# Performance work log

Measured on AMD Instinct MI355X. Metric: run time of the kernel, lower is better.

The kernel has to match this reference:

```python
import jax, jax.numpy as jnp
from jax import lax
import numpy as np

B, C, H, Wd = 32, 128, 56, 56
FILTERS = 128
KH = KW = 3
T_MIN_PREV = 0.0  # module defaults (set_params never called)
T_MIN = 0.0
T_MAX = 1.0


def setup_inputs() -> dict:
    key = jax.random.key(0)
    k1, k2 = jax.random.split(key)
    tj = jax.random.uniform(k1, (B, C, H, Wd), dtype=jnp.float32)          # spike times
    W = jax.random.normal(k2, (C * KH * KW, FILTERS), dtype=jnp.float32) * 0.02  # kernel.view(-1, filters)
    D_i = jnp.zeros((9, FILTERS), dtype=jnp.float32)                        # intrinsic delays (only row 0 used)
    return {"tj": tj, "W": W, "D_i": D_i}


def reference(tj, W, D_i):
    # 'same' padding with value t_min, then unfold + (tj - t_min) @ W is
    # exactly a zero-padded conv on (tj - t_min): the pad entries become 0.
    x = tj - T_MIN                                   # [B,C,H,W]
    # Unfold orders patch rows as (C, kh, kw); build the equivalent OIHW kernel.
    kernel = jnp.transpose(W.reshape(C, KH, KW, FILTERS), (3, 0, 1, 2))  # [F,C,KH,KW]
    y = lax.conv_general_dilated(
        x, kernel, window_strides=(1, 1), padding="SAME",
        dimension_numbers=("NCHW", "OIHW", "NCHW"))    # [B,F,H,W]
    threshold = T_MAX - T_MIN - D_i[0]                 # [F]
    ti = y + threshold[None, :, None, None] + T_MIN
    ti = jnp.minimum(ti, T_MAX)                        # torch.where(ti < t_max, ti, t_max)
    return jnp.transpose(ti, (0, 2, 3, 1))             # [B,H,W,F], matches ti.view(b,H,W,filters)
```

## Files before the change

kernel.cpp:

```cpp
#include <hip/hip_runtime.h>


#define BZ 32
#define CC 128
#define HH 56
#define WWD 56
#define HWP 3136
#define FF 128
#define KT 9
#define PH 58
#define PW 58
#define MTOT 100352
#define BM 128

typedef __attribute__((ext_vector_type(8))) __bf16 bf16x8;
typedef __attribute__((ext_vector_type(4))) float f32x4;
typedef __attribute__((ext_vector_type(8))) unsigned short us8;
typedef __attribute__((ext_vector_type(4))) float flt4;

__device__ __forceinline__ unsigned short f2bf(float f) {
  unsigned int u = __float_as_uint(f);
  unsigned int r = (u + 0x7FFFu + ((u >> 16) & 1u)) >> 16;
  return (unsigned short)r;
}

#define GLOAD_LDS16(g, l)                                                              \
  __builtin_amdgcn_global_load_lds((const __attribute__((address_space(1))) void*)(g), \
                                   (__attribute__((address_space(3))) void*)(l), 16, 0, 0)

__global__ void prep_w_kernel(const float* __restrict__ W, unsigned short* __restrict__ Wt,
                              int swz) {
  int idx = blockIdx.x * 256 + threadIdx.x;
  if (idx >= KT * FF * CC) return;
  int r = idx >> 14;
  int rem = idx & 16383;
  int f = rem >> 7;
  int c = rem & 127;
  int cs = swz ? (c ^ ((f & 7) << 3)) : c;
  Wt[(r * FF + f) * CC + cs] = f2bf(W[(c * KT + r) * FF + f]);
}

__global__ __launch_bounds__(256) void prep_x_kernel(const float* __restrict__ x,
                                                     unsigned short* __restrict__ xp) {
  const int blk = blockIdx.x;
  const int b = blk / PH;
  const int ph = blk - b * PH;
  const int tid = threadIdx.x;
  unsigned short* dst = xp + (size_t)(b * PH + ph) * PW * CC;

  if (ph == 0 || ph == PH - 1) {
    us8 z;
#pragma unroll
    for (int k = 0; k < 8; ++k) z[k] = 0;
    for (int i = tid; i < PW * CC / 8; i += 256) reinterpret_cast<us8*>(dst)[i] = z;
    return;
  }

  __shared__ float sm[CC][57];
  const int h = ph - 1;
  {
    const int c = tid >> 1;
    const int half = tid & 1;
    const float* src = x + ((size_t)(b * CC + c)) * HWP + h * WWD + half * 28;
#pragma unroll
    for (int k = 0; k < 7; ++k) {
      flt4 v = *reinterpret_cast<const flt4*>(src + k * 4);
      sm[c][half * 28 + k * 4 + 0] = v[0];
      sm[c][half * 28 + k * 4 + 1] = v[1];
      sm[c][half * 28 + k * 4 + 2] = v[2];
      sm[c][half * 28 + k * 4 + 3] = v[3];
    }
  }
  __syncthreads();
  for (int i = tid; i < PW * 16; i += 256) {
    const int ww = i >> 4;
    const int cg = i & 15;
    us8 v;
    if (ww == 0 || ww == PW - 1) {
#pragma unroll
      for (int k = 0; k < 8; ++k) v[k] = 0;
    } else {
      const int w = ww - 1;
#pragma unroll
      for (int k = 0; k < 8; ++k) v[k] = f2bf(sm[cg * 8 + k][w]);
    }
    reinterpret_cast<us8*>(dst)[i] = v;
  }
}

__global__ __launch_bounds__(256, 2) void spiking_conv_main(
    const unsigned short* __restrict__ xp, const unsigned short* __restrict__ Wt,
    const float* __restrict__ Di, float* __restrict__ out) {
  __shared__ unsigned short Asm[BM * CC];
  __shared__ unsigned short Bsm[FF * CC];

  const int bid = blockIdx.x;
  const int wg = (bid & 7) * 98 + (bid >> 3);
  const int m0 = wg * BM;

  const int tid = threadIdx.x;
  const int lane = tid & 63;
  const int wv = tid >> 6;
  const int wr = wv >> 1, wc = wv & 1;
  const int frow = lane & 15, kg = lane >> 4;

  int aoff[8];
#pragma unroll
  for (int t = 0; t < 8; ++t) {
    const int row = wv * 32 + t * 4 + (lane >> 4);
    const int m = m0 + row;
    const int b = m / HWP;
    const int p = m - b * HWP;
    const int h = p / WWD;
    const int w = p - h * WWD;
    const int chunk = (lane & 15) ^ (row & 7);
    aoff[t] = ((b * PH + h + 1) * PW + (w + 1)) * CC + chunk * 8;
  }
  const unsigned short* wsrc = Wt + wv * 4096 + lane * 8;

  f32x4 acc[4][4];
  const f32x4 zero = {0.0f, 0.0f, 0.0f, 0.0f};
#pragma unroll
  for (int i = 0; i < 4; ++i)
#pragma unroll
    for (int j = 0; j < 4; ++j) acc[i][j] = zero;

  for (int r = 0; r < KT; ++r) {
    const int dh = r / 3 - 1;
    const int dw = r - (r / 3) * 3 - 1;
    const int tapoff = (dh * PW + dw) * CC;
    __syncthreads();
#pragma unroll
    for (int t = 0; t < 8; ++t)
      GLOAD_LDS16(xp + aoff[t] + tapoff, Asm + wv * 4096 + t * 512);
#pragma unroll
    for (int t = 0; t < 8; ++t)
      GLOAD_LDS16(wsrc + r * (FF * CC) + t * 512, Bsm + wv * 4096 + t * 512);
    __syncthreads();

#pragma unroll
    for (int kk = 0; kk < 4; ++kk) {
      bf16x8 af[4], bfr[4];
#pragma unroll
      for (int i = 0; i < 4; ++i) {
        const int rowA = wr * 64 + i * 16 + frow;
        const int colb = (kk * 64 + kg * 16) ^ ((rowA & 7) << 4);
        af[i] = *reinterpret_cast<const bf16x8*>(
            reinterpret_cast<const char*>(Asm) + rowA * 256 + colb);
      }
#pragma unroll
      for (int j = 0; j < 4; ++j) {
        const int rowB = wc * 64 + j * 16 + frow;
        const int colb = (kk * 64 + kg * 16) ^ ((rowB & 7) << 4);
        bfr[j] = *reinterpret_cast<const bf16x8*>(
            reinterpret_cast<const char*>(Bsm) + rowB * 256 + colb);
      }
#pragma unroll
      for (int i = 0; i < 4; ++i)
#pragma unroll
        for (int j = 0; j < 4; ++j)
          acc[i][j] = __builtin_amdgcn_mfma_f32_16x16x32_bf16(af[i], bfr[j], acc[i][j], 0, 0, 0);
    }
  }

#pragma unroll
  for (int j = 0; j < 4; ++j) {
    const int col = wc * 64 + j * 16 + frow;
    const float thr = 1.0f - Di[col];
#pragma unroll
    for (int i = 0; i < 4; ++i) {
      const int rbase = m0 + wr * 64 + i * 16 + kg * 4;
#pragma unroll
      for (int q = 0; q < 4; ++q) {
        float v = acc[i][j][q] + thr;
        out[(size_t)(rbase + q) * FF + col] = fminf(v, 1.0f);
      }
    }
  }
}

__global__ __launch_bounds__(256) void spiking_conv_fallback(
    const float* __restrict__ x, const unsigned short* __restrict__ Wt,
    const float* __restrict__ Wf, const float* __restrict__ Di,
    float* __restrict__ out, int useWt) {
  __shared__ unsigned short Asm2[BM][32];
  __shared__ unsigned short Bsm2[FF][32];
  const int tid = threadIdx.x;
  const int m0 = blockIdx.x * BM;
  const int mi = tid & 127;
  const int half = tid >> 7;
  const int m = m0 + mi;
  const int bimg = m / HWP;
  const int p = m - bimg * HWP;
  const int h = p / WWD;
  const int w = p - h * WWD;
  const int baseA = (bimg * CC) * HWP + h * WWD + w;
  const int lane = tid & 63;
  const int wid = tid >> 6;
  const int wr = wid >> 1;
  const int wc = wid & 1;
  const int frow = lane & 15;
  const int kg = lane >> 4;
  f32x4 acc[4][4];
  const f32x4 zero = {0.0f, 0.0f, 0.0f, 0.0f};
#pragma unroll
  for (int i = 0; i < 4; ++i)
#pragma unroll
    for (int j = 0; j < 4; ++j) acc[i][j] = zero;
  for (int r = 0; r < KT; ++r) {
    const int dh = r / 3 - 1;
    const int dw = r - (r / 3) * 3 - 1;
    const int hh = h + dh;
    const int ww2 = w + dw;
    const bool valid = ((unsigned)hh < (unsigned)HH) && ((unsigned)ww2 < (unsigned)WWD);
    const int aoff2 = baseA + dh * WWD + dw + half * 16 * HWP;
    for (int c0 = 0; c0 < CC; c0 += 32) {
      __syncthreads();
      {
        const float* src = x + aoff2 + c0 * HWP;
        us8 v0, v1;
#pragma unroll
        for (int i = 0; i < 8; ++i) {
          float f0 = valid ? src[i * HWP] : 0.0f;
          float f1 = valid ? src[(i + 8) * HWP] : 0.0f;
          v0[i] = f2bf(f0);
          v1[i] = f2bf(f1);
        }
        *reinterpret_cast<us8*>(&Asm2[mi][half * 16]) = v0;
        *reinterpret_cast<us8*>(&Asm2[mi][half * 16 + 8]) = v1;
      }
      if (useWt) {
        const unsigned short* src = Wt + (r * FF + mi) * CC + c0 + half * 16;
        *reinterpret_cast<us8*>(&Bsm2[mi][half * 16]) = *reinterpret_cast<const us8*>(src);
        *reinterpret_cast<us8*>(&Bsm2[mi][half * 16 + 8]) = *reinterpret_cast<const us8*>(src + 8);
      } else {
        us8 v0, v1;
#pragma unroll
        for (int i = 0; i < 8; ++i) {
          int c = c0 + half * 16 + i;
          v0[i] = f2bf(Wf[(c * KT + r) * FF + mi]);
          v1[i] = f2bf(Wf[((c + 8) * KT + r) * FF + mi]);
        }
        *reinterpret_cast<us8*>(&Bsm2[mi][half * 16]) = v0;
        *reinterpret_cast<us8*>(&Bsm2[mi][half * 16 + 8]) = v1;
      }
      __syncthreads();
      bf16x8 af[4], bfr[4];
#pragma unroll
      for (int i = 0; i < 4; ++i)
        af[i] = *reinterpret_cast<const bf16x8*>(&Asm2[wr * 64 + i * 16 + frow][kg * 8]);
#pragma unroll
      for (int j = 0; j < 4; ++j)
        bfr[j] = *reinterpret_cast<const bf16x8*>(&Bsm2[wc * 64 + j * 16 + frow][kg * 8]);
#pragma unroll
      for (int i = 0; i < 4; ++i)
#pragma unroll
        for (int j = 0; j < 4; ++j)
          acc[i][j] = __builtin_amdgcn_mfma_f32_16x16x32_bf16(af[i], bfr[j], acc[i][j], 0, 0, 0);
    }
  }
#pragma unroll
  for (int j = 0; j < 4; ++j) {
    const int col = wc * 64 + j * 16 + frow;
    const float thr = 1.0f - Di[col];
#pragma unroll
    for (int i = 0; i < 4; ++i) {
      const int rbase = m0 + wr * 64 + i * 16 + kg * 4;
#pragma unroll
      for (int q = 0; q < 4; ++q) {
        float v = acc[i][j][q] + thr;
        out[(size_t)(rbase + q) * FF + col] = fminf(v, 1.0f);
      }
    }
  }
}

extern "C" void kernel_launch(void* const* d_in, const int* in_sizes, int n_in,
                              void* d_out, int out_size, void* d_ws, size_t ws_size,
                              hipStream_t stream) {
  const float* tj = (const float*)d_in[0];
  const float* W = (const float*)d_in[1];
  const float* Di = (const float*)d_in[2];
  float* out = (float*)d_out;

  const size_t wt_bytes = (size_t)KT * FF * CC * 2;
  const size_t xp_bytes = (size_t)BZ * PH * PW * CC * 2;
  unsigned short* Wt = (unsigned short*)d_ws;
  unsigned short* xp = (unsigned short*)((char*)d_ws + wt_bytes);

  if (ws_size >= wt_bytes + xp_bytes) {
    prep_w_kernel<<<(KT * FF * CC + 255) / 256, 256, 0, stream>>>(W, Wt, 1);
    prep_x_kernel<<<BZ * PH, 256, 0, stream>>>(tj, xp);
    spiking_conv_main<<<MTOT / BM, 256, 0, stream>>>(xp, Wt, Di, out);
  } else {
    const int useWt = (ws_size >= wt_bytes) ? 1 : 0;
    if (useWt) prep_w_kernel<<<(KT * FF * CC + 255) / 256, 256, 0, stream>>>(W, Wt, 0);
    spiking_conv_fallback<<<MTOT / BM, 256, 0, stream>>>(tj, Wt, W, Di, out, useWt);
  }
}
```

Baseline: 66.15 us.

## Tile conv by spatial row blocks with shared halo patch and pipelined K-steps

The main conv kernel now assigns each 512-thread workgroup an 8-row spatial tile of one image. It loads one padded halo patch per 32-channel quarter into LDS and reuses it for all 9 taps by shifting addresses, instead of reloading A for every tap. Weights are re-laid out per (quarter, tap) step and double-buffered. The 36 steps are fully unrolled via templates, with prefetch of the next step overlapped with MFMA. This cuts redundant global A traffic and barrier stalls, at the cost of 96KB dynamic LDS, a large accumulator register footprint (7x4 tiles), and only 224 workgroups.

New measurement: 58.40 us. 1.13x faster.

```diff
diff --git a/kernel.cpp b/kernel.cpp
--- a/kernel.cpp
+++ b/kernel.cpp
@@ -7,11 +7,15 @@
 #define WWD 56
 #define HWP 3136
 #define FF 128
-#define KT 9
 #define PH 58
 #define PW 58
-#define MTOT 100352
-#define BM 128
+#define QC 32
+#define PATCH_G 2320
+#define PATCH_BYTES 40960
+#define BQ_OFF 81920
+#define BQ_BYTES 8192
+#define LDS_TOTAL 98304
+#define NSTEP 36
 
 typedef __attribute__((ext_vector_type(8))) __bf16 bf16x8;
 typedef __attribute__((ext_vector_type(4))) float f32x4;
@@ -28,16 +32,21 @@
   __builtin_amdgcn_global_load_lds((const __attribute__((address_space(1))) void*)(g), \
                                    (__attribute__((address_space(3))) void*)(l), 16, 0, 0)
 
-__global__ void prep_w_kernel(const float* __restrict__ W, unsigned short* __restrict__ Wt,
-                              int swz) {
+__global__ void prep_w_kernel(const float* __restrict__ W, unsigned short* __restrict__ Wt) {
   int idx = blockIdx.x * 256 + threadIdx.x;
-  if (idx >= KT * FF * CC) return;
-  int r = idx >> 14;
-  int rem = idx & 16383;
-  int f = rem >> 7;
-  int c = rem & 127;
-  int cs = swz ? (c ^ ((f & 7) << 3)) : c;
-  Wt[(r * FF + f) * CC + cs] = f2bf(W[(c * KT + r) * FF + f]);
+  if (idx >= 4 * 9 * 512) return;
+  int qr = idx >> 9;
+  int gp = idx & 511;
+  int g = gp ^ ((gp >> 3) & 7);
+  int q = qr / 9, r = qr - q * 9;
+  int f = g >> 2, kg = g & 3;
+  us8 v;
+#pragma unroll
+  for (int j = 0; j < 8; ++j) {
+    int c = q * QC + kg * 8 + j;
+    v[j] = f2bf(W[(c * 9 + r) * FF + f]);
+  }
+  *reinterpret_cast<us8*>(Wt + (size_t)idx * 8) = v;
 }
 
 __global__ __launch_bounds__(256) void prep_x_kernel(const float* __restrict__ x,
@@ -88,105 +97,155 @@
   }
 }
 
-__global__ __launch_bounds__(256, 2) void spiking_conv_main(
+struct Ctx {
+  const unsigned short* xp;
+  const unsigned short* Wt;
+  int tid;
+  int srcA[5];
+  int gbase[7];
+  int bOffB[4];
+  f32x4 acc[7][4];
+};
+
+template <int S>
+__device__ __forceinline__ void step(Ctx& c, unsigned char* lds) {
+  constexpr int q = S / 9, r = S - q * 9;
+  constexpr int dh = r / 3 - 1, dw = r - (r / 3) * 3 - 1;
+  constexpr int tapoff = dh * 232 + dw * 4;
+  constexpr bool issueA = (r < 5) && (q < 3);
+  constexpr bool issueB = (S < NSTEP - 1);
+  constexpr int nIssue = (issueA ? 1 : 0) + (issueB ? 1 : 0);
+
+  if constexpr (issueA) {
+    const unsigned short* src = c.xp + c.srcA[r] + (q + 1) * QC;
+    unsigned char* dst = lds + ((q + 1) & 1) * PATCH_BYTES + (size_t)(r * 512 + c.tid) * 16;
+    GLOAD_LDS16(src, dst);
+  }
+  if constexpr (issueB) {
+    const unsigned short* src = c.Wt + (size_t)(S + 1) * 4096 + c.tid * 8;
+    unsigned char* dst = lds + BQ_OFF + ((S + 1) & 1) * BQ_BYTES + (size_t)c.tid * 16;
+    GLOAD_LDS16(src, dst);
+  }
+  asm volatile("s_waitcnt vmcnt(%0)" ::"n"(nIssue));
+  __builtin_amdgcn_s_barrier();
+  __builtin_amdgcn_sched_barrier(0);
+
+  const unsigned char* pa = lds + (q & 1) * PATCH_BYTES;
+  const unsigned char* pb = lds + BQ_OFF + (S & 1) * BQ_BYTES;
+  bf16x8 af[7], bf[4];
+#pragma unroll
+  for (int i = 0; i < 7; ++i) {
+    int g = c.gbase[i] + tapoff;
+    int ga = (g ^ ((g >> 3) & 7)) << 4;
+    af[i] = *reinterpret_cast<const bf16x8*>(pa + ga);
+  }
+#pragma unroll
+  for (int j = 0; j < 4; ++j)
+    bf[j] = *reinterpret_cast<const bf16x8*>(pb + c.bOffB[j]);
+
+  __builtin_amdgcn_s_setprio(1);
+#pragma unroll
+  for (int i = 0; i < 7; ++i)
+#pragma unroll
+    for (int j = 0; j < 4; ++j)
+      c.acc[i][j] = __builtin_amdgcn_mfma_f32_16x16x32_bf16(af[i], bf[j], c.acc[i][j], 0, 0, 0);
+  __builtin_amdgcn_s_setprio(0);
+  __builtin_amdgcn_sched_barrier(0);
+  __builtin_amdgcn_s_barrier();
+}
+
+template <int S>
+__device__ __forceinline__ void do_steps(Ctx& c, unsigned char* lds) {
+  step<S>(c, lds);
+  if constexpr (S + 1 < NSTEP) do_steps<S + 1>(c, lds);
+}
+
+__global__ __launch_bounds__(512, 2) void spiking_conv_main(
     const unsigned short* __restrict__ xp, const unsigned short* __restrict__ Wt,
     const float* __restrict__ Di, float* __restrict__ out) {
-  __shared__ unsigned short Asm[BM * CC];
-  __shared__ unsigned short Bsm[FF * CC];
+  extern __shared__ unsigned char lds[];
 
   const int bid = blockIdx.x;
-  const int wg = (bid & 7) * 98 + (bid >> 3);
-  const int m0 = wg * BM;
-
+  const int wg = (bid & 7) * 28 + (bid >> 3);
+  const int b = wg / 7;
+  const int ht = wg - b * 7;
+  const int h0 = ht * 8;
+
+  Ctx c;
+  c.xp = xp;
+  c.Wt = Wt;
   const int tid = threadIdx.x;
-  const int lane = tid & 63;
-  const int wv = tid >> 6;
+  c.tid = tid;
+  const int lane = tid & 63, wv = tid >> 6;
   const int wr = wv >> 1, wc = wv & 1;
   const int frow = lane & 15, kg = lane >> 4;
 
-  int aoff[8];
-#pragma unroll
-  for (int t = 0; t < 8; ++t) {
-    const int row = wv * 32 + t * 4 + (lane >> 4);
-    const int m = m0 + row;
-    const int b = m / HWP;
-    const int p = m - b * HWP;
-    const int h = p / WWD;
-    const int w = p - h * WWD;
-    const int chunk = (lane & 15) ^ (row & 7);
-    aoff[t] = ((b * PH + h + 1) * PW + (w + 1)) * CC + chunk * 8;
-  }
-  const unsigned short* wsrc = Wt + wv * 4096 + lane * 8;
-
-  f32x4 acc[4][4];
+#pragma unroll
+  for (int k = 0; k < 5; ++k) {
+    int gp = k * 512 + tid;
+    int g = gp ^ ((gp >> 3) & 7);
+    int ph = g / 232;
+    int rem = g - ph * 232;
+    int pw = rem >> 2;
+    int kg2 = rem & 3;
+    int e = ((b * PH + h0 + ph) * PW + pw) * CC + kg2 * 8;
+    c.srcA[k] = (gp < PATCH_G) ? e : 0;
+  }
+#pragma unroll
+  for (int i = 0; i < 7; ++i) {
+    int t = 16 * i + frow;
+    int hl = (t >= 56) ? 1 : 0;
+    int wl = t - 56 * hl;
+    c.gbase[i] = ((2 * wr + hl + 1) * 58 + (wl + 1)) * 4 + kg;
+  }
+#pragma unroll
+  for (int j = 0; j < 4; ++j) {
+    int gB = (wc * 64 + 16 * j + frow) * 4 + kg;
+    c.bOffB[j] = (gB ^ ((gB >> 3) & 7)) << 4;
+  }
   const f32x4 zero = {0.0f, 0.0f, 0.0f, 0.0f};
 #pragma unroll
-  for (int i = 0; i < 4; ++i)
-#pragma unroll
-    for (int j = 0; j < 4; ++j) acc[i][j] = zero;
-
-  for (int r = 0; r < KT; ++r) {
-    const int dh = r / 3 - 1;
-    const int dw = r - (r / 3) * 3 - 1;
-    const int tapoff = (dh * PW + dw) * CC;
-    __syncthreads();
-#pragma unroll
-    for (int t = 0; t < 8; ++t)
-      GLOAD_LDS16(xp + aoff[t] + tapoff, Asm + wv * 4096 + t * 512);
-#pragma unroll
-    for (int t = 0; t < 8; ++t)
-      GLOAD_LDS16(wsrc + r * (FF * CC) + t * 512, Bsm + wv * 4096 + t * 512);
-    __syncthreads();
-
-#pragma unroll
-    for (int kk = 0; kk < 4; ++kk) {
-      bf16x8 af[4], bfr[4];
-#pragma unroll
-      for (int i = 0; i < 4; ++i) {
-        const int rowA = wr * 64 + i * 16 + frow;
-        const int colb = (kk * 64 + kg * 16) ^ ((rowA & 7) << 4);
-        af[i] = *reinterpret_cast<const bf16x8*>(
-            reinterpret_cast<const char*>(Asm) + rowA * 256 + colb);
+  for (int i = 0; i < 7; ++i)
+#pragma unroll
+    for (int j = 0; j < 4; ++j) c.acc[i][j] = zero;
+
+#pragma unroll
+  for (int k = 0; k < 5; ++k)
+    GLOAD_LDS16(xp + c.srcA[k], lds + (size_t)(k * 512 + tid) * 16);
+  GLOAD_LDS16(Wt + tid * 8, lds + BQ_OFF + (size_t)tid * 16);
+  asm volatile("s_waitcnt vmcnt(0)");
+  __builtin_amdgcn_s_barrier();
+  __builtin_amdgcn_sched_barrier(0);
+
+  do_steps<0>(c, lds);
+
+#pragma unroll
+  for (int j = 0; j < 4; ++j) {
+    const int col = wc * 64 + 16 * j + frow;
+    const float thr = 1.0f - Di[col];
+#pragma unroll
+    for (int i = 0; i < 7; ++i) {
+      const int bt = 16 * i + kg * 4;
+      const int hl = (bt >= 56) ? 1 : 0;
+      const int wl0 = bt - 56 * hl;
+      const int orow = h0 + 2 * wr + hl;
+      const size_t obase = ((size_t)b * HWP + (size_t)orow * WWD + wl0) * FF + col;
+#pragma unroll
+      for (int qq = 0; qq < 4; ++qq) {
+        float v = c.acc[i][j][qq] + thr;
+        out[obase + (size_t)qq * FF] = fminf(v, 1.0f);
       }
-#pragma unroll
-      for (int j = 0; j < 4; ++j) {
-        const int rowB = wc * 64 + j * 16 + frow;
-        const int colb = (kk * 64 + kg * 16) ^ ((rowB & 7) << 4);
-        bfr[j] = *reinterpret_cast<const bf16x8*>(
-            reinterpret_cast<const char*>(Bsm) + rowB * 256 + colb);
-      }
-#pragma unroll
-      for (int i = 0; i < 4; ++i)
-#pragma unroll
-        for (int j = 0; j < 4; ++j)
-          acc[i][j] = __builtin_amdgcn_mfma_f32_16x16x32_bf16(af[i], bfr[j], acc[i][j], 0, 0, 0);
-    }
-  }
-
-#pragma unroll
-  for (int j = 0; j < 4; ++j) {
-    const int col = wc * 64 + j * 16 + frow;
-    const float thr = 1.0f - Di[col];
-#pragma unroll
-    for (int i = 0; i < 4; ++i) {
-      const int rbase = m0 + wr * 64 + i * 16 + kg * 4;
-#pragma unroll
-      for (int q = 0; q < 4; ++q) {
-        float v = acc[i][j][q] + thr;
-        out[(size_t)(rbase + q) * FF + col] = fminf(v, 1.0f);
-      }
     }
   }
 }
 
 __global__ __launch_bounds__(256) void spiking_conv_fallback(
-    const float* __restrict__ x, const unsigned short* __restrict__ Wt,
-    const float* __restrict__ Wf, const float* __restrict__ Di,
-    float* __restrict__ out, int useWt) {
-  __shared__ unsigned short Asm2[BM][32];
-  __shared__ unsigned short Bsm2[FF][32];
+    const float* __restrict__ x, const float* __restrict__ Wf,
+    const float* __restrict__ Di, float* __restrict__ out) {
+  __shared__ unsigned short Asm2[128][32];
+  __shared__ unsigned short Bsm2[128][32];
   const int tid = threadIdx.x;
-  const int m0 = blockIdx.x * BM;
+  const int m0 = blockIdx.x * 128;
   const int mi = tid & 127;
   const int half = tid >> 7;
   const int m = m0 + mi;
@@ -207,7 +266,7 @@
   for (int i = 0; i < 4; ++i)
 #pragma unroll
     for (int j = 0; j < 4; ++j) acc[i][j] = zero;
-  for (int r = 0; r < KT; ++r) {
+  for (int r = 0; r < 9; ++r) {
     const int dh = r / 3 - 1;
     const int dw = r - (r / 3) * 3 - 1;
     const int hh = h + dh;
@@ -229,17 +288,13 @@
         *reinterpret_cast<us8*>(&Asm2[mi][half * 16]) = v0;
         *reinterpret_cast<us8*>(&Asm2[mi][half * 16 + 8]) = v1;
       }
-      if (useWt) {
-        const unsigned short* src = Wt + (r * FF + mi) * CC + c0 + half * 16;
-        *reinterpret_cast<us8*>(&Bsm2[mi][half * 16]) = *reinterpret_cast<const us8*>(src);
-        *reinterpret_cast<us8*>(&Bsm2[mi][half * 16 + 8]) = *reinterpret_cast<const us8*>(src + 8);
-      } else {
+      {
         us8 v0, v1;
 #pragma unroll
         for (int i = 0; i < 8; ++i) {
-          int c = c0 + half * 16 + i;
-          v0[i] = f2bf(Wf[(c * KT + r) * FF + mi]);
-          v1[i] = f2bf(Wf[((c + 8) * KT + r) * FF + mi]);
+          int cc2 = c0 + half * 16 + i;
+          v0[i] = f2bf(Wf[(cc2 * 9 + r) * FF + mi]);
+          v1[i] = f2bf(Wf[((cc2 + 8) * 9 + r) * FF + mi]);
         }
         *reinterpret_cast<us8*>(&Bsm2[mi][half * 16]) = v0;
         *reinterpret_cast<us8*>(&Bsm2[mi][half * 16 + 8]) = v1;
@@ -267,9 +322,9 @@
     for (int i = 0; i < 4; ++i) {
       const int rbase = m0 + wr * 64 + i * 16 + kg * 4;
 #pragma unroll
-      for (int q = 0; q < 4; ++q) {
-        float v = acc[i][j][q] + thr;
-        out[(size_t)(rbase + q) * FF + col] = fminf(v, 1.0f);
+      for (int qq = 0; qq < 4; ++qq) {
+        float v = acc[i][j][qq] + thr;
+        out[(size_t)(rbase + qq) * FF + col] = fminf(v, 1.0f);
       }
     }
   }
@@ -283,18 +338,19 @@
   const float* Di = (const float*)d_in[2];
   float* out = (float*)d_out;
 
-  const size_t wt_bytes = (size_t)KT * FF * CC * 2;
+  const size_t wt_bytes = (size_t)4 * 9 * 512 * 16;
   const size_t xp_bytes = (size_t)BZ * PH * PW * CC * 2;
   unsigned short* Wt = (unsigned short*)d_ws;
   unsigned short* xp = (unsigned short*)((char*)d_ws + wt_bytes);
 
-  if (ws_size >= wt_bytes + xp_bytes) {
-    prep_w_kernel<<<(KT * FF * CC + 255) / 256, 256, 0, stream>>>(W, Wt, 1);
+  bool fast = (ws_size >= wt_bytes + xp_bytes);
+  if (fast) {
+    prep_w_kernel<<<72, 256, 0, stream>>>(W, Wt);
     prep_x_kernel<<<BZ * PH, 256, 0, stream>>>(tj, xp);
-    spiking_conv_main<<<MTOT / BM, 256, 0, stream>>>(xp, Wt, Di, out);
-  } else {
-    const int useWt = (ws_size >= wt_bytes) ? 1 : 0;
-    if (useWt) prep_w_kernel<<<(KT * FF * CC + 255) / 256, 256, 0, stream>>>(W, Wt, 0);
-    spiking_conv_fallback<<<MTOT / BM, 256, 0, stream>>>(tj, Wt, W, Di, out, useWt);
-  }
-}
+    spiking_conv_main<<<224, 512, LDS_TOTAL, stream>>>(xp, Wt, Di, out);
+    if (hipGetLastError() != hipSuccess) fast = false;
+  }
+  if (!fast) {
+    spiking_conv_fallback<<<100352 / 128, 256, 0, stream>>>(tj, W, Di, out);
+  }
+}
```
